# Performance work log

Hardware: AMD Instinct MI355X
Metric: run time of the kernel (lower is better)

Reference implementation:

```python
import jax, jax.numpy as jnp
import numpy as np

# --- SLAYER-style constants (network.yaml defaults) ---
T_BINS = 350      # tSample / Ts
TS = 1.0          # simulation time step
THETA = 10.0      # spike threshold
TAU_SR = 10.0     # SRM (psp) kernel time constant
TAU_REF = 1.0     # refractory kernel time constant
SCALE_REF = 2.0
TAU_RHO = 1.0     # surrogate-gradient width (unused in fwd)
SCALE_RHO = 1.0
REF_LEN = 32      # truncated refractory kernel length
B = 32            # batch

_t = jnp.arange(T_BINS, dtype=jnp.float32) * TS
SRM_KERNEL = (_t / TAU_SR) * jnp.exp(1.0 - _t / TAU_SR)            # alpha kernel, peak 1 at t=tauSr
_tr = jnp.arange(REF_LEN, dtype=jnp.float32) * TS
REF_KERNEL = -SCALE_REF * THETA * (_tr / TAU_REF) * jnp.exp(1.0 - _tr / TAU_REF)


def psp(x):
    # causal temporal convolution with SRM kernel; x: [B, N, T]
    b, n, t = x.shape
    k = SRM_KERNEL[::-1].reshape(1, 1, T_BINS)  # flip: lax conv is cross-correlation
    y = jax.lax.conv_general_dilated(x.reshape(b * n, 1, t), k, (1,), [(T_BINS - 1, 0)])
    return y.reshape(b, n, t)


def _spike_fwd_impl(u):
    # threshold + refractory dynamics, serial over time; u: [B, N, T]
    uT = jnp.moveaxis(u, -1, 0)  # [T, B, N]
    def step(buf, ut):
        v = ut + buf[..., 0]                       # membrane + pending refractory
        s = (v >= THETA).astype(u.dtype)           # 0/1 spike indicator
        buf = jnp.concatenate([buf[..., 1:], jnp.zeros_like(buf[..., :1])], axis=-1) \
              + s[..., None] * REF_KERNEL
        return buf, s / TS
    buf0 = jnp.zeros(u.shape[:-1] + (REF_LEN,), u.dtype)
    _, sT = jax.lax.scan(step, buf0, uT)
    return jnp.moveaxis(sT, 0, -1)


@jax.custom_vjp
def spike(u):
    return _spike_fwd_impl(u)

def _spike_f(u):
    return _spike_fwd_impl(u), u

def _spike_b(u, g):
    # SLAYER surrogate gradient: pdf of spiking
    pdf = (SCALE_RHO / TAU_RHO) * jnp.exp(-jnp.abs(u - THETA) / TAU_RHO)
    return (g * pdf,)

spike.defvjp(_spike_f, _spike_b)


def encode(inp, table):
    # vectorized pixel->time-bin one-hot scatter (replaces the Python quadruple loop)
    t_idx = table[inp]                                   # gather: [B,3,32,32]
    return jax.nn.one_hot(t_idx, T_BINS, dtype=jnp.float32) / TS  # [B,3,32,32,T]


def setup_inputs() -> dict:
    key = jax.random.key(0)
    k1, k2, k3 = jax.random.split(key, 3)
    inp = jax.random.randint(k1, (B, 3, 32, 32), 0, 256, dtype=jnp.int32)
    table = ((jnp.arange(256) * T_BINS) // 256).astype(jnp.int32)  # pixel value -> time bin
    w1 = jax.random.normal(k2, (240, 3 * 32 * 32), dtype=jnp.float32)
    w2 = jax.random.normal(k3, (10, 240), dtype=jnp.float32)
    return {"inp": inp, "table": table, "w1": w1, "w2": w2}


def reference(inp, table, w1, w2):
    spikes = encode(inp, table).reshape(inp.shape[0], -1, T_BINS)      # [B,3072,T]
    l1 = spike(psp(jnp.einsum('bpt,np->bnt', spikes, w1)))             # [B,240,T]
    l2 = spike(psp(jnp.einsum('bpt,np->bnt', l1, w2)))                 # [B,10,T]
    return l2
```

## Files before the change

### kernel.cpp

```cpp
#include <hip/hip_runtime.h>
#include <math.h>

#define T_BINS 350
#define REF_LEN 32
#define NB 32
#define NPIX 3072
#define N1 240
#define N2 10
#define NVAL 256
#define WROW 256
#define WROWS (NVAL + 1)
#define CH 14
#define NCHUNK 25

__global__ void prep(const int* __restrict__ inp,
                     int* __restrict__ pix,
                     int* __restrict__ offs,
                     int* __restrict__ cnts,
                     const float* __restrict__ w1,
                     float* __restrict__ w1t,
                     const int* __restrict__ table,
                     int* __restrict__ inv)
{
    __shared__ int lc[NVAL];
    __shared__ int ls[NVAL];
    __shared__ int lslot[NVAL];
    __shared__ float tile[64][65];
    __shared__ int linv[T_BINS];

    const int tid = threadIdx.x;

    if (blockIdx.x < NB) {
        const int b = blockIdx.x;
        lc[tid] = 0;
        __syncthreads();

        int vals[12];
        #pragma unroll
        for (int i = 0; i < 12; ++i) {
            int v = inp[b * NPIX + i * 256 + tid];
            vals[i] = v;
            atomicAdd(&lc[v], 1);
        }
        __syncthreads();

        int x = lc[tid];
        ls[tid] = x;
        __syncthreads();
        for (int d = 1; d < 256; d <<= 1) {
            int y = (tid >= d) ? ls[tid - d] : 0;
            __syncthreads();
            ls[tid] += y;
            __syncthreads();
        }
        int excl = ls[tid] - x;
        offs[b * NVAL + tid] = excl;
        cnts[b * NVAL + tid] = x;
        lslot[tid] = excl;
        __syncthreads();

        #pragma unroll
        for (int i = 0; i < 12; ++i) {
            int slot = atomicAdd(&lslot[vals[i]], 1);
            pix[b * NPIX + slot] = i * 256 + tid;
        }
    } else if (blockIdx.x < NB + 192) {
        const int tt = blockIdx.x - NB;
        const int p0 = (tt % 48) * 64;
        const int n0 = (tt / 48) * 64;
        const int c  = tid & 63;
        const int r0 = tid >> 6;

        #pragma unroll
        for (int i = 0; i < 16; ++i) {
            int n = n0 + r0 + i * 4;
            if (n < N1) tile[r0 + i * 4][c] = w1[n * NPIX + p0 + c];
        }
        __syncthreads();
        #pragma unroll
        for (int i = 0; i < 16; ++i) {
            int p = p0 + r0 + i * 4;
            int n = n0 + c;
            if (n < N1) w1t[p * N1 + n] = tile[c][r0 + i * 4];
        }
    } else {
        for (int i = tid; i < T_BINS; i += 256) linv[i] = -1;
        __syncthreads();
        if (tid < NVAL) linv[table[tid]] = tid;
        __syncthreads();
        for (int i = tid; i < T_BINS; i += 256) inv[i] = linv[i];
    }
}

__global__ void compute_w(const float* __restrict__ w1t,
                          const int* __restrict__ pix,
                          const int* __restrict__ offs,
                          const int* __restrict__ cnts,
                          float* __restrict__ W)
{
    const int v   = blockIdx.x;
    const int b   = blockIdx.y;
    const int tid = threadIdx.x;

    float outv = 0.0f;
    if (tid < N1) {
        const int cnt = cnts[b * NVAL + v];
        const int* pl = pix + b * NPIX + offs[b * NVAL + v];
        double acc = 0.0;
        int i = 0;
        for (; i + 4 <= cnt; i += 4) {
            int p0 = pl[i], p1 = pl[i + 1], p2 = pl[i + 2], p3 = pl[i + 3];
            double w0  = (double)w1t[p0 * N1 + tid];
            double w1v = (double)w1t[p1 * N1 + tid];
            double w2v = (double)w1t[p2 * N1 + tid];
            double w3  = (double)w1t[p3 * N1 + tid];
            acc += w0; acc += w1v; acc += w2v; acc += w3;
        }
        for (; i < cnt; ++i)
            acc += (double)w1t[pl[i] * N1 + tid];
        outv = (float)acc;
    }
    W[((size_t)b * WROWS + v) * WROW + tid] = outv;
    if (v == 0)
        W[((size_t)b * WROWS + NVAL) * WROW + tid] = 0.0f;
}

#define DYN_CONSTS \
    const double A    = 0.9048374180359595;     \
    const double C    = 0.2718281828459045;     \
    const double Ar   = 0.36787944117144233;    \
    const double Cr   = -54.365636569180904;    \
    const double C31A = 1.0671679036256927e-12; \
    const double C31B = 3.4424771084699765e-14;

#define DYN_CORE(uin)                                         \
        q = A * (q + p);                                      \
        p = A * p + (uin);                                    \
        double vm = C * q + Cr * Q;                           \
        unsigned int sb = (vm >= 10.0) ? 1u : 0u;             \
        double s = (double)sb;                                \
        double sel31 = (hist & 0x80000000u) ? C31A : 0.0;     \
        double sel30 = (hist & 0x40000000u) ? C31B : 0.0;     \
        Q = Ar * (Q + P - sel31);                             \
        P = s + (Ar * P - sel30);                             \
        hist = (hist << 1) | sb;

#define F14(M) M(0) M(1) M(2) M(3) M(4) M(5) M(6) M(7) M(8) M(9) M(10) M(11) M(12) M(13)

__global__ __launch_bounds__(512, 1) void fused_dyn(
        const float* __restrict__ W,
        const int* __restrict__ inv,
        const float* __restrict__ w2,
        float* __restrict__ out)
{
    __shared__ unsigned long long mbuf[2][CH][4];
    __shared__ float u2buf[2][CH][11];
    __shared__ float sout[T_BINS][11];
    __shared__ float lw2[N2][N1 + 1];
    __shared__ int loff[T_BINS];

    const int tid  = threadIdx.x;
    const int b    = blockIdx.x;
    const int wid  = tid >> 6;
    const int lane = tid & 63;

    for (int i = tid; i < N2 * N1; i += 512) lw2[i / N1][i % N1] = w2[i];
    for (int i = tid; i < T_BINS; i += 512) {
        int v = inv[i];
        loff[i] = ((v >= 0) ? v : NVAL) * (WROW * 4);
    }
    __syncthreads();

    DYN_CONSTS
    double p = 0.0, q = 0.0, P = 0.0, Q = 0.0;
    unsigned int hist = 0u;

#define DECL_CF(i) float c##i = 0.0f, f##i = 0.0f;
    F14(DECL_CF)

    const char* wb = nullptr;
    if (wid < 4) {
        const int n = wid * 64 + lane;
        wb = (const char*)W + ((size_t)b * WROWS) * (WROW * 4) + (size_t)n * 4;
#define LOADC(i) c##i = *(const float*)(wb + loff[i]);
        F14(LOADC)
    }

    for (int it = 0; it < NCHUNK + 2; ++it) {
        if (wid < 4 && it < NCHUNK) {
            if (it + 1 < NCHUNK) {
                const int base = (it + 1) * CH;
#define LOADF(i) f##i = *(const float*)(wb + loff[base + i]);
                F14(LOADF)
            }
            const int slot = it & 1;
#define STEP1(i) { DYN_CORE((double)c##i)                                  \
                   unsigned long long msk = __ballot(sb != 0u);            \
                   if (lane == 0) mbuf[slot][i][wid] = msk; }
            F14(STEP1)
            asm volatile("" : "+v"(f0), "+v"(f1), "+v"(f2), "+v"(f3),
                              "+v"(f4), "+v"(f5), "+v"(f6), "+v"(f7),
                              "+v"(f8), "+v"(f9), "+v"(f10), "+v"(f11),
                              "+v"(f12), "+v"(f13));
#define COPYC(i) c##i = f##i;
            F14(COPYC)
        } else if (wid >= 4 && wid < 7 && it >= 1 && it <= NCHUNK) {
            const int item = (wid - 4) * 64 + lane;
            if (item < CH * N2) {
                const int st = item / N2;
                const int m  = item - st * N2;
                const int slot = (it - 1) & 1;
                double acc = 0.0;
                #pragma unroll
                for (int kk = 0; kk < 4; ++kk) {
                    unsigned long long msk = mbuf[slot][st][kk];
                    while (msk) {
                        int j = __ffsll(msk) - 1;
                        acc += (double)lw2[m][kk * 64 + j];
                        msk &= msk - 1;
                    }
                }
                u2buf[slot][st][m] = (float)acc;
            }
        } else if (wid == 7 && lane < N2 && it >= 2) {
            const int cl = it - 2;
            const int slot = cl & 1;
            const int m = lane;
            const int tb = cl * CH;
#define DECL_G(i) float g##i = u2buf[slot][i][m];
            F14(DECL_G)
            asm volatile("" : "+v"(g0), "+v"(g1), "+v"(g2), "+v"(g3),
                              "+v"(g4), "+v"(g5), "+v"(g6), "+v"(g7),
                              "+v"(g8), "+v"(g9), "+v"(g10), "+v"(g11),
                              "+v"(g12), "+v"(g13));
#define STEP3(i) { DYN_CORE((double)g##i) sout[tb + i][m] = (float)s; }
            F14(STEP3)
        }
        __syncthreads();
    }

    float* ob = out + (size_t)b * N2 * T_BINS;
    for (int id = tid; id < N2 * T_BINS; id += 512) {
        const int m = id / T_BINS;
        const int t = id - m * T_BINS;
        ob[id] = sout[t][m];
    }
}

extern "C" void kernel_launch(void* const* d_in, const int* in_sizes, int n_in,
                              void* d_out, int out_size, void* d_ws, size_t ws_size,
                              hipStream_t stream) {
    const int*   inp   = (const int*)d_in[0];
    const int*   table = (const int*)d_in[1];
    const float* w1    = (const float*)d_in[2];
    const float* w2    = (const float*)d_in[3];
    float* out = (float*)d_out;

    char* ws = (char*)d_ws;
    size_t off = 0;
    float* W   = (float*)(ws + off);  off += (size_t)NB * WROWS * WROW * 4;
    float* w1t = (float*)(ws + off);  off += (size_t)NPIX * N1 * 4;
    int*   pix = (int*)(ws + off);    off += (size_t)NB * NPIX * 4;
    int*  offs = (int*)(ws + off);    off += (size_t)NB * NVAL * 4;
    int*  cnts = (int*)(ws + off);    off += (size_t)NB * NVAL * 4;
    int*   inv = (int*)(ws + off);    off += (size_t)T_BINS * 4;

    prep<<<NB + 192 + 1, 256, 0, stream>>>(inp, pix, offs, cnts, w1, w1t, table, inv);
    compute_w<<<dim3(NVAL, NB), 256, 0, stream>>>(w1t, pix, offs, cnts, W);
    fused_dyn<<<NB, 512, 0, stream>>>(W, inv, w2, out);
}
```

Measured before the change: 142.6 us.

## Fuse three kernels into one cooperative kernel with grid-wide syncs

Merges the prep, compute_w and dynamics kernels into a single cooperative launch of 256 blocks of 512 threads. The phases are separated by grid.sync() instead of kernel boundaries, so two launch gaps are removed. The W computation is spread as 16 tasks per half-block, and blocks beyond the batch exit before the serial dynamics phase. In exchange, grid barriers have their own cost. The single-occupancy launch bound and the larger shared memory footprint also constrain scheduling.

```diff
diff --git a/kernel.cpp b/kernel.cpp
--- a/kernel.cpp
+++ b/kernel.cpp
@@ -1,5 +1,8 @@
 #include <hip/hip_runtime.h>
+#include <hip/hip_cooperative_groups.h>
 #include <math.h>
+
+namespace cg = cooperative_groups;
 
 #define T_BINS 350
 #define REF_LEN 32
@@ -12,118 +15,7 @@
 #define WROWS (NVAL + 1)
 #define CH 14
 #define NCHUNK 25
-
-__global__ void prep(const int* __restrict__ inp,
-                     int* __restrict__ pix,
-                     int* __restrict__ offs,
-                     int* __restrict__ cnts,
-                     const float* __restrict__ w1,
-                     float* __restrict__ w1t,
-                     const int* __restrict__ table,
-                     int* __restrict__ inv)
-{
-    __shared__ int lc[NVAL];
-    __shared__ int ls[NVAL];
-    __shared__ int lslot[NVAL];
-    __shared__ float tile[64][65];
-    __shared__ int linv[T_BINS];
-
-    const int tid = threadIdx.x;
-
-    if (blockIdx.x < NB) {
-        const int b = blockIdx.x;
-        lc[tid] = 0;
-        __syncthreads();
-
-        int vals[12];
-        #pragma unroll
-        for (int i = 0; i < 12; ++i) {
-            int v = inp[b * NPIX + i * 256 + tid];
-            vals[i] = v;
-            atomicAdd(&lc[v], 1);
-        }
-        __syncthreads();
-
-        int x = lc[tid];
-        ls[tid] = x;
-        __syncthreads();
-        for (int d = 1; d < 256; d <<= 1) {
-            int y = (tid >= d) ? ls[tid - d] : 0;
-            __syncthreads();
-            ls[tid] += y;
-            __syncthreads();
-        }
-        int excl = ls[tid] - x;
-        offs[b * NVAL + tid] = excl;
-        cnts[b * NVAL + tid] = x;
-        lslot[tid] = excl;
-        __syncthreads();
-
-        #pragma unroll
-        for (int i = 0; i < 12; ++i) {
-            int slot = atomicAdd(&lslot[vals[i]], 1);
-            pix[b * NPIX + slot] = i * 256 + tid;
-        }
-    } else if (blockIdx.x < NB + 192) {
-        const int tt = blockIdx.x - NB;
-        const int p0 = (tt % 48) * 64;
-        const int n0 = (tt / 48) * 64;
-        const int c  = tid & 63;
-        const int r0 = tid >> 6;
-
-        #pragma unroll
-        for (int i = 0; i < 16; ++i) {
-            int n = n0 + r0 + i * 4;
-            if (n < N1) tile[r0 + i * 4][c] = w1[n * NPIX + p0 + c];
-        }
-        __syncthreads();
-        #pragma unroll
-        for (int i = 0; i < 16; ++i) {
-            int p = p0 + r0 + i * 4;
-            int n = n0 + c;
-            if (n < N1) w1t[p * N1 + n] = tile[c][r0 + i * 4];
-        }
-    } else {
-        for (int i = tid; i < T_BINS; i += 256) linv[i] = -1;
-        __syncthreads();
-        if (tid < NVAL) linv[table[tid]] = tid;
-        __syncthreads();
-        for (int i = tid; i < T_BINS; i += 256) inv[i] = linv[i];
-    }
-}
-
-__global__ void compute_w(const float* __restrict__ w1t,
-                          const int* __restrict__ pix,
-                          const int* __restrict__ offs,
-                          const int* __restrict__ cnts,
-                          float* __restrict__ W)
-{
-    const int v   = blockIdx.x;
-    const int b   = blockIdx.y;
-    const int tid = threadIdx.x;
-
-    float outv = 0.0f;
-    if (tid < N1) {
-        const int cnt = cnts[b * NVAL + v];
-        const int* pl = pix + b * NPIX + offs[b * NVAL + v];
-        double acc = 0.0;
-        int i = 0;
-        for (; i + 4 <= cnt; i += 4) {
-            int p0 = pl[i], p1 = pl[i + 1], p2 = pl[i + 2], p3 = pl[i + 3];
-            double w0  = (double)w1t[p0 * N1 + tid];
-            double w1v = (double)w1t[p1 * N1 + tid];
-            double w2v = (double)w1t[p2 * N1 + tid];
-            double w3  = (double)w1t[p3 * N1 + tid];
-            acc += w0; acc += w1v; acc += w2v; acc += w3;
-        }
-        for (; i < cnt; ++i)
-            acc += (double)w1t[pl[i] * N1 + tid];
-        outv = (float)acc;
-    }
-    W[((size_t)b * WROWS + v) * WROW + tid] = outv;
-    if (v == 0)
-        W[((size_t)b * WROWS + NVAL) * WROW + tid] = 0.0f;
-}
+#define GRID_BLOCKS 256
 
 #define DYN_CONSTS \
     const double A    = 0.9048374180359595;     \
@@ -147,20 +39,142 @@
 
 #define F14(M) M(0) M(1) M(2) M(3) M(4) M(5) M(6) M(7) M(8) M(9) M(10) M(11) M(12) M(13)
 
-__global__ __launch_bounds__(512, 1) void fused_dyn(
-        const float* __restrict__ W,
-        const int* __restrict__ inv,
+__global__ __launch_bounds__(512, 1) void snn_all(
+        const int* __restrict__ inp,
+        const int* __restrict__ table,
+        const float* __restrict__ w1,
         const float* __restrict__ w2,
-        float* __restrict__ out)
+        float* __restrict__ out,
+        float* __restrict__ W,
+        float* __restrict__ w1t,
+        int* __restrict__ pix,
+        int* __restrict__ offs,
+        int* __restrict__ cnts,
+        int* __restrict__ inv)
 {
+    cg::grid_group grid = cg::this_grid();
+
+    __shared__ int lc[NVAL];
+    __shared__ int ls[NVAL];
+    __shared__ int lslot[NVAL];
+    __shared__ float tile[64][65];
+    __shared__ int linv[T_BINS];
     __shared__ unsigned long long mbuf[2][CH][4];
     __shared__ float u2buf[2][CH][11];
     __shared__ float sout[T_BINS][11];
     __shared__ float lw2[N2][N1 + 1];
     __shared__ int loff[T_BINS];
 
-    const int tid  = threadIdx.x;
-    const int b    = blockIdx.x;
+    const int tid = threadIdx.x;
+    const int bx  = blockIdx.x;
+
+    if (bx < NB) {
+        const int b = bx;
+        if (tid < NVAL) lc[tid] = 0;
+        __syncthreads();
+
+        int vals[12];
+        if (tid < 256) {
+            #pragma unroll
+            for (int i = 0; i < 12; ++i) {
+                int v = inp[b * NPIX + i * 256 + tid];
+                vals[i] = v;
+                atomicAdd(&lc[v], 1);
+            }
+        }
+        __syncthreads();
+
+        int x = 0;
+        if (tid < 256) { x = lc[tid]; ls[tid] = x; }
+        __syncthreads();
+        for (int d = 1; d < 256; d <<= 1) {
+            int y = 0;
+            if (tid < 256) y = (tid >= d) ? ls[tid - d] : 0;
+            __syncthreads();
+            if (tid < 256) ls[tid] += y;
+            __syncthreads();
+        }
+        if (tid < 256) {
+            int excl = ls[tid] - x;
+            offs[b * NVAL + tid] = excl;
+            cnts[b * NVAL + tid] = x;
+            lslot[tid] = excl;
+        }
+        __syncthreads();
+
+        if (tid < 256) {
+            #pragma unroll
+            for (int i = 0; i < 12; ++i) {
+                int slot = atomicAdd(&lslot[vals[i]], 1);
+                pix[b * NPIX + slot] = i * 256 + tid;
+            }
+        }
+    } else if (bx < NB + 192) {
+        const int tt = bx - NB;
+        const int p0 = (tt % 48) * 64;
+        const int n0 = (tt / 48) * 64;
+        const int c  = tid & 63;
+        const int r0 = tid >> 6;
+
+        #pragma unroll
+        for (int i = 0; i < 8; ++i) {
+            int row = r0 + i * 8;
+            int n = n0 + row;
+            if (n < N1) tile[row][c] = w1[n * NPIX + p0 + c];
+        }
+        __syncthreads();
+        #pragma unroll
+        for (int i = 0; i < 8; ++i) {
+            int row = r0 + i * 8;
+            int p = p0 + row;
+            int n = n0 + c;
+            if (n < N1) w1t[p * N1 + n] = tile[c][row];
+        }
+    } else if (bx == NB + 192) {
+        for (int i = tid; i < T_BINS; i += 512) linv[i] = -1;
+        __syncthreads();
+        if (tid < NVAL) linv[table[tid]] = tid;
+        __syncthreads();
+        for (int i = tid; i < T_BINS; i += 512) inv[i] = linv[i];
+    }
+
+    grid.sync();
+
+    if (bx < NB && tid < 256)
+        W[((size_t)bx * WROWS + NVAL) * WROW + tid] = 0.0f;
+    {
+        const int half = tid >> 8;
+        const int col  = tid & 255;
+        for (int r = 0; r < 16; ++r) {
+            const int task = bx * 32 + half * 16 + r;
+            const int b = task >> 8;
+            const int v = task & 255;
+            float outv = 0.0f;
+            if (col < N1) {
+                const int cnt = cnts[b * NVAL + v];
+                const int* pl = pix + b * NPIX + offs[b * NVAL + v];
+                double acc = 0.0;
+                int i = 0;
+                for (; i + 4 <= cnt; i += 4) {
+                    int p0 = pl[i], p1 = pl[i + 1], p2 = pl[i + 2], p3 = pl[i + 3];
+                    double w0  = (double)w1t[p0 * N1 + col];
+                    double w1v = (double)w1t[p1 * N1 + col];
+                    double w2v = (double)w1t[p2 * N1 + col];
+                    double w3  = (double)w1t[p3 * N1 + col];
+                    acc += w0; acc += w1v; acc += w2v; acc += w3;
+                }
+                for (; i < cnt; ++i)
+                    acc += (double)w1t[pl[i] * N1 + col];
+                outv = (float)acc;
+            }
+            W[((size_t)b * WROWS + v) * WROW + col] = outv;
+        }
+    }
+
+    grid.sync();
+
+    if (bx >= NB) return;
+    const int b    = bx;
     const int wid  = tid >> 6;
     const int lane = tid & 63;
 
@@ -265,7 +279,10 @@
     int*  cnts = (int*)(ws + off);    off += (size_t)NB * NVAL * 4;
     int*   inv = (int*)(ws + off);    off += (size_t)T_BINS * 4;
 
-    prep<<<NB + 192 + 1, 256, 0, stream>>>(inp, pix, offs, cnts, w1, w1t, table, inv);
-    compute_w<<<dim3(NVAL, NB), 256, 0, stream>>>(w1t, pix, offs, cnts, W);
-    fused_dyn<<<NB, 512, 0, stream>>>(W, inv, w2, out);
+    void* args[] = { (void*)&inp, (void*)&table, (void*)&w1, (void*)&w2,
+                     (void*)&out, (void*)&W, (void*)&w1t,
+                     (void*)&pix, (void*)&offs, (void*)&cnts, (void*)&inv };
+    hipLaunchCooperativeKernel((const void*)snn_all,
+                               dim3(GRID_BLOCKS), dim3(512),
+                               args, 0, stream);
 }
```

Result: slower. 242.9 us (+70.4%).
